# Optimization experiments

Hardware: AMD Instinct MI355X
Metric: run time of the kernel (lower is better)

The kernel has to match this reference:

```python
import jax, jax.numpy as jnp
import numpy as np

K = 8
W_CONST = 0.01
EPS = 1e-8


def _normalize(v, eps=1e-8):
    return v / (jnp.linalg.norm(v, axis=-1, keepdims=True) + eps)


def _coarse_normal(x, vertices, vertex_normals):
    # x: (N,3); vertices, vertex_normals: (V,3)
    # brute-force KNN (ascending by squared distance, like cKDTree.query)
    d2_all = jnp.sum((x[:, None, :] - vertices[None, :, :]) ** 2, axis=-1)  # (N,V)
    neg_d2, idx = jax.lax.top_k(-d2_all, K)  # sorted ascending distance
    d2 = -neg_d2                                                    # (N,K)
    v_knn = vertices[idx]                                           # (N,K,3)
    n_knn = vertex_normals[idx]                                     # (N,K,3)
    d2c = jnp.maximum(d2, EPS)
    inv_d2 = 1.0 / d2c                                              # (N,K)
    term_knn = jnp.sum(n_knn * inv_d2[..., None], axis=1)           # (N,3)
    v1 = v_knn[:, 0]                                                # nearest vertex
    d2_v1 = jnp.maximum(jnp.sum((x - v1) ** 2, axis=-1), EPS)       # (N,)
    term_dir = (x - v1) / (W_CONST * d2_v1[:, None])
    W = jnp.sum(inv_d2, axis=1) + 1.0 / W_CONST                     # (N,)
    n_tilde = (term_knn + term_dir) / W[:, None]
    nc = _normalize(n_tilde)
    return nc, v1


def _ray_mesh_first_hit(origins, dirs, tri0, e1, e2):
    # Moller-Trumbore, all points vs all faces. origins/dirs: (N,3); tri0/e1/e2: (F,3)
    pvec = jnp.cross(dirs[:, None, :], e2[None, :, :])              # (N,F,3)
    det = jnp.einsum('fk,nfk->nf', e1, pvec)                        # (N,F)
    ok_det = jnp.abs(det) > EPS
    inv_det = jnp.where(ok_det, 1.0 / jnp.where(ok_det, det, 1.0), 0.0)
    tvec = origins[:, None, :] - tri0[None, :, :]                   # (N,F,3)
    u = jnp.sum(tvec * pvec, axis=-1) * inv_det
    qvec = jnp.cross(tvec, e1[None, :, :])                          # (N,F,3)
    v = jnp.einsum('nk,nfk->nf', dirs, qvec) * inv_det
    t = jnp.einsum('fk,nfk->nf', e2, qvec) * inv_det
    valid = ok_det & (u >= 0.0) & (v >= 0.0) & (u + v <= 1.0) & (t > EPS)
    t_masked = jnp.where(valid, t, jnp.inf)
    t_min = jnp.min(t_masked, axis=1)                               # first hit along ray
    hit = jnp.isfinite(t_min)
    loc = origins + dirs * jnp.where(hit, t_min, 0.0)[:, None]
    return hit, loc


def _project(x, vertices, vertex_normals, faces):
    nc, v1 = _coarse_normal(x, vertices, vertex_normals)
    tri0 = vertices[faces[:, 0]]
    e1 = vertices[faces[:, 1]] - tri0
    e2 = vertices[faces[:, 2]] - tri0
    # primary cast along -nc
    hit1, loc1 = _ray_mesh_first_hit(x, -nc, tri0, e1, e2)
    # fallback cast toward nearest vertex
    dir_fb = _normalize(v1 - x)
    hit2, loc2 = _ray_mesh_first_hit(x, dir_fb, tri0, e1, e2)
    xc = jnp.where(hit1[:, None], loc1, jnp.where(hit2[:, None], loc2, v1))
    s = jnp.sum((x - xc) * nc, axis=-1, keepdims=True)              # (N,1)
    return xc, s, nc


def setup_inputs() -> dict:
    key = jax.random.key(0)
    k1, k2, k3, k4 = jax.random.split(key, 4)
    N, V, F = 2048, 8192, 8192
    x = jax.random.normal(k1, (N, 3), dtype=jnp.float32)
    vertices = jax.random.normal(k2, (V, 3), dtype=jnp.float32)
    vertex_normals = _normalize(jax.random.normal(k3, (V, 3), dtype=jnp.float32))
    faces = jax.random.randint(k4, (F, 3), 0, V, dtype=jnp.int32)
    return {"x": x, "vertices": vertices, "vertex_normals": vertex_normals, "faces": faces}


def reference(x, vertices, vertex_normals, faces):
    # returns (xc:(N,3), s:(N,1), nc:(N,3)) like ProjectionFn.forward
    return _project(x, vertices, vertex_normals, faces)
```

## Files before the change

kernel.cpp:

```cpp
#include <hip/hip_runtime.h>
#include <math.h>

#pragma float_control(precise, on)

#define EPSF 1e-8f
#define TRI_CHUNK 64


__global__ void __launch_bounds__(256) knn_kernel(
    const float* __restrict__ x, const float* __restrict__ verts,
    const float* __restrict__ vnorm, float* __restrict__ ncw,
    float* __restrict__ v1w, float* __restrict__ dfbw,
    unsigned int* __restrict__ tmin, int N, int V) {
#pragma clang fp contract(off)
    int p = blockIdx.x;
    int tid = threadIdx.x;
    int wave = tid >> 6;
    int lane = tid & 63;
    if (p >= N) return;

    if (tid < 2) tmin[2 * p + tid] = 0x7f800000u;

    float xx = x[p * 3 + 0];
    float xy = x[p * 3 + 1];
    float xz = x[p * 3 + 2];

    unsigned long long ka[8], kb[8];
#pragma unroll
    for (int i = 0; i < 8; ++i) { ka[i] = ~0ULL; kb[i] = ~0ULL; }

    for (int va = tid; va < V; va += 512) {
        int vb = va + 256;
        bool hasB = vb < V;

        float avx = verts[va * 3 + 0];
        float avy = verts[va * 3 + 1];
        float avz = verts[va * 3 + 2];
        float bvx = 0.f, bvy = 0.f, bvz = 0.f;
        if (hasB) {
            bvx = verts[vb * 3 + 0];
            bvy = verts[vb * 3 + 1];
            bvz = verts[vb * 3 + 2];
        }

        float dxa = xx - avx, dya = xy - avy, dza = xz - avz;
        float d2a = ((dxa * dxa) + (dya * dya)) + (dza * dza);
        unsigned long long kA =
            (((unsigned long long)__float_as_uint(d2a)) << 32) | (unsigned int)va;
        if (kA < ka[7]) {
            ka[7] = kA;
#pragma unroll
            for (int j = 7; j > 0; --j) {
                if (ka[j] < ka[j - 1]) {
                    unsigned long long t = ka[j];
                    ka[j] = ka[j - 1];
                    ka[j - 1] = t;
                }
            }
        }

        if (hasB) {
            float dxb = xx - bvx, dyb = xy - bvy, dzb = xz - bvz;
            float d2b = ((dxb * dxb) + (dyb * dyb)) + (dzb * dzb);
            unsigned long long kB =
                (((unsigned long long)__float_as_uint(d2b)) << 32) | (unsigned int)vb;
            if (kB < kb[7]) {
                kb[7] = kB;
#pragma unroll
                for (int j = 7; j > 0; --j) {
                    if (kb[j] < kb[j - 1]) {
                        unsigned long long t = kb[j];
                        kb[j] = kb[j - 1];
                        kb[j - 1] = t;
                    }
                }
            }
        }
    }

    unsigned long long wsel[8];
#pragma unroll
    for (int j = 0; j < 8; ++j) {
        unsigned long long c = (ka[0] < kb[0]) ? ka[0] : kb[0];
        unsigned long long m = c;
#pragma unroll
        for (int s = 1; s < 64; s <<= 1) {
            unsigned long long o = __shfl_xor(m, s, 64);
            if (o < m) m = o;
        }
        if (c == m) {
            if (ka[0] == m) {
#pragma unroll
                for (int t = 0; t < 7; ++t) ka[t] = ka[t + 1];
                ka[7] = ~0ULL;
            } else {
#pragma unroll
                for (int t = 0; t < 7; ++t) kb[t] = kb[t + 1];
                kb[7] = ~0ULL;
            }
        }
        wsel[j] = m;
    }

    __shared__ unsigned long long cand[32];
    if (lane == 0) {
#pragma unroll
        for (int j = 0; j < 8; ++j) cand[wave * 8 + j] = wsel[j];
    }
    __syncthreads();
    if (wave != 0) return;

    unsigned long long c0 = (lane < 32) ? cand[lane] : ~0ULL;
    unsigned long long sel[8];
#pragma unroll
    for (int j = 0; j < 8; ++j) {
        unsigned long long m = c0;
#pragma unroll
        for (int s = 1; s < 64; s <<= 1) {
            unsigned long long o = __shfl_xor(m, s, 64);
            if (o < m) m = o;
        }
        if (c0 == m) c0 = ~0ULL;
        sel[j] = m;
    }

    if (lane != 0) return;

    float invk[8];
    float nsx = 0.f, nsy = 0.f, nsz = 0.f;
#pragma unroll
    for (int j = 0; j < 8; ++j) {
        int id = (int)(sel[j] & 0xffffffffu);
        float d2 = __uint_as_float((unsigned int)(sel[j] >> 32));
        float inv = 1.0f / fmaxf(d2, EPSF);
        invk[j] = inv;
        nsx = nsx + vnorm[id * 3 + 0] * inv;
        nsy = nsy + vnorm[id * 3 + 1] * inv;
        nsz = nsz + vnorm[id * 3 + 2] * inv;
    }
    float Wsum = ((invk[0] + invk[1]) + (invk[2] + invk[3])) +
                 ((invk[4] + invk[5]) + (invk[6] + invk[7]));

    int id0 = (int)(sel[0] & 0xffffffffu);
    float v1x = verts[id0 * 3 + 0];
    float v1y = verts[id0 * 3 + 1];
    float v1z = verts[id0 * 3 + 2];

    float dxv = xx - v1x, dyv = xy - v1y, dzv = xz - v1z;
    float d2v1 = fmaxf(((dxv * dxv) + (dyv * dyv)) + (dzv * dzv), EPSF);
    float den = 0.01f * d2v1;
    float tdx = dxv / den, tdy = dyv / den, tdz = dzv / den;

    float W = Wsum + 100.0f;
    float ntx = (nsx + tdx) / W;
    float nty = (nsy + tdy) / W;
    float ntz = (nsz + tdz) / W;
    float nrm = sqrtf(((ntx * ntx) + (nty * nty)) + (ntz * ntz)) + 1e-8f;
    float ncx = ntx / nrm, ncy = nty / nrm, ncz = ntz / nrm;

    float fx = v1x - xx, fy = v1y - xy, fz = v1z - xz;
    float fn = sqrtf(((fx * fx) + (fy * fy)) + (fz * fz)) + 1e-8f;
    fx = fx / fn; fy = fy / fn; fz = fz / fn;

    ncw[p * 3 + 0] = ncx; ncw[p * 3 + 1] = ncy; ncw[p * 3 + 2] = ncz;
    v1w[p * 3 + 0] = v1x; v1w[p * 3 + 1] = v1y; v1w[p * 3 + 2] = v1z;
    dfbw[p * 3 + 0] = fx; dfbw[p * 3 + 1] = fy; dfbw[p * 3 + 2] = fz;
}

__global__ void __launch_bounds__(256) ray_kernel(
    const float* __restrict__ x, const float* __restrict__ ncw,
    const float* __restrict__ dfbw, const float* __restrict__ verts,
    const int* __restrict__ faces,
    unsigned int* __restrict__ tmin, int N, int F) {
#pragma clang fp contract(off)
    const float M = 1e-5f;
    __shared__ __align__(16) float sh[TRI_CHUNK * 12];
    int tid = threadIdx.x;
    int cbase = blockIdx.y * TRI_CHUNK;
    int cnt = min(TRI_CHUNK, F - cbase);

    for (int j = tid; j < cnt; j += 256) {
        int fi = cbase + j;
        int f0 = faces[fi * 3 + 0];
        int f1 = faces[fi * 3 + 1];
        int f2 = faces[fi * 3 + 2];
        float t0x = verts[f0 * 3 + 0], t0y = verts[f0 * 3 + 1], t0z = verts[f0 * 3 + 2];
        float ax = verts[f1 * 3 + 0], ay = verts[f1 * 3 + 1], az = verts[f1 * 3 + 2];
        float bx = verts[f2 * 3 + 0], by = verts[f2 * 3 + 1], bz = verts[f2 * 3 + 2];
        float4* s4 = (float4*)(sh + j * 12);
        s4[0] = make_float4(t0x, t0y, t0z, ax - t0x);
        s4[1] = make_float4(ay - t0y, az - t0z, bx - t0x, by - t0y);
        sh[j * 12 + 8] = bz - t0z;
    }
    __syncthreads();

    int rid = blockIdx.x * 256 + tid;
    if (rid >= 2 * N) return;
    int pnt = rid >> 1;

    float ox = x[pnt * 3 + 0];
    float oy = x[pnt * 3 + 1];
    float oz = x[pnt * 3 + 2];
    float dx, dy, dz;
    if (rid & 1) {
        dx = dfbw[pnt * 3 + 0]; dy = dfbw[pnt * 3 + 1]; dz = dfbw[pnt * 3 + 2];
    } else {
        dx = -ncw[pnt * 3 + 0]; dy = -ncw[pnt * 3 + 1]; dz = -ncw[pnt * 3 + 2];
    }

    const float INF = __uint_as_float(0x7f800000u);
    float tbest = INF;
    for (int j = 0; j < cnt; ++j) {
        const float4 A = *(const float4*)(sh + j * 12);
        const float4 B = *(const float4*)(sh + j * 12 + 4);
        const float e2z = sh[j * 12 + 8];
        float e1x = A.w, e1y = B.x, e1z = B.y;
        float e2x = B.z, e2y = B.w;
        float px = (dy * e2z) - (dz * e2y);
        float py = (dz * e2x) - (dx * e2z);
        float pz = (dx * e2y) - (dy * e2x);
        float det = ((e1x * px) + (e1y * py)) + (e1z * pz);
        bool ok = fabsf(det) > EPSF;
        float inv = ok ? (1.0f / det) : 0.0f;
        float tvx = ox - A.x;
        float tvy = oy - A.y;
        float tvz = oz - A.z;
        float u = (((tvx * px) + (tvy * py)) + (tvz * pz)) * inv;
        float qx = (tvy * e1z) - (tvz * e1y);
        float qy = (tvz * e1x) - (tvx * e1z);
        float qz = (tvx * e1y) - (tvy * e1x);
        float v = (((dx * qx) + (dy * qy)) + (dz * qz)) * inv;
        float t = (((e2x * qx) + (e2y * qy)) + (e2z * qz)) * inv;
        bool valid = ok && (u >= -M) && (v >= -M) && ((u + v) <= 1.0f + M) && (t > EPSF);
        tbest = (valid && t < tbest) ? t : tbest;
    }
    if (tbest < INF) atomicMin(&tmin[rid], __float_as_uint(tbest));
}

__global__ void finalize_kernel(const float* __restrict__ x,
                                const float* __restrict__ ncw,
                                const float* __restrict__ v1w,
                                const float* __restrict__ dfbw,
                                const unsigned int* __restrict__ tmin,
                                float* __restrict__ out, int N) {
#pragma clang fp contract(off)
    int p = blockIdx.x * blockDim.x + threadIdx.x;
    if (p >= N) return;
    float t1 = __uint_as_float(tmin[2 * p + 0]);
    float t2 = __uint_as_float(tmin[2 * p + 1]);
    bool h1 = t1 < __uint_as_float(0x7f800000u);
    bool h2 = t2 < __uint_as_float(0x7f800000u);

    float xx = x[p * 3 + 0], xy = x[p * 3 + 1], xz = x[p * 3 + 2];
    float ncx = ncw[p * 3 + 0], ncy = ncw[p * 3 + 1], ncz = ncw[p * 3 + 2];

    float xcx, xcy, xcz;
    if (h1) {
        xcx = xx + ((-ncx) * t1);
        xcy = xy + ((-ncy) * t1);
        xcz = xz + ((-ncz) * t1);
    } else if (h2) {
        xcx = xx + (dfbw[p * 3 + 0] * t2);
        xcy = xy + (dfbw[p * 3 + 1] * t2);
        xcz = xz + (dfbw[p * 3 + 2] * t2);
    } else {
        xcx = v1w[p * 3 + 0]; xcy = v1w[p * 3 + 1]; xcz = v1w[p * 3 + 2];
    }
    float s = (((xx - xcx) * ncx) + ((xy - xcy) * ncy)) + ((xz - xcz) * ncz);

    out[p * 3 + 0] = xcx;
    out[p * 3 + 1] = xcy;
    out[p * 3 + 2] = xcz;
    out[3 * N + p] = s;
    out[4 * N + p * 3 + 0] = ncx;
    out[4 * N + p * 3 + 1] = ncy;
    out[4 * N + p * 3 + 2] = ncz;
}

extern "C" void kernel_launch(void* const* d_in, const int* in_sizes, int n_in,
                              void* d_out, int out_size, void* d_ws, size_t ws_size,
                              hipStream_t stream) {
    const float* x     = (const float*)d_in[0];
    const float* verts = (const float*)d_in[1];
    const float* vnorm = (const float*)d_in[2];
    const int*   faces = (const int*)d_in[3];
    int N = in_sizes[0] / 3;
    int V = in_sizes[1] / 3;
    int F = in_sizes[3] / 3;

    unsigned int* tmin = (unsigned int*)d_ws;
    float* ncw  = (float*)(tmin + 2 * N);
    float* v1w  = ncw + 3 * N;
    float* dfbw = v1w + 3 * N;

    hipLaunchKernelGGL(knn_kernel, dim3(N), dim3(256), 0, stream,
                       x, verts, vnorm, ncw, v1w, dfbw, tmin, N, V);
    int chunks = (F + TRI_CHUNK - 1) / TRI_CHUNK;
    int rblocks = (2 * N + 255) / 256;
    hipLaunchKernelGGL(ray_kernel, dim3(rblocks, chunks), dim3(256), 0, stream,
                       x, ncw, dfbw, verts, faces, tmin, N, F);
    hipLaunchKernelGGL(finalize_kernel, dim3((N + 255) / 256), dim3(256), 0, stream,
                       x, ncw, v1w, dfbw, tmin, (float*)d_out, N);
}
```

Baseline: 157.9 us.

## Process both rays per point in one thread, sharing tvec and qvec work

Each thread now handles one point and tests both of its rays (primary and fallback) against every triangle in the chunk. The direction-independent tvec, qvec and the t numerator are computed once and reused for both rays, and shared-memory triangle loads are amortized over two rays. The triangle chunk is halved to keep the block count up, and a launch-bounds occupancy hint is added. In exchange each thread uses more registers, there are more chunks and atomics overall, and only half as many threads work per chunk.

```diff
diff --git a/kernel.cpp b/kernel.cpp
--- a/kernel.cpp
+++ b/kernel.cpp
@@ -4,7 +4,7 @@
 #pragma float_control(precise, on)
 
 #define EPSF 1e-8f
-#define TRI_CHUNK 64
+#define TRI_CHUNK 32
 
 
 __global__ void __launch_bounds__(256) knn_kernel(
@@ -167,7 +167,7 @@
     dfbw[p * 3 + 0] = fx; dfbw[p * 3 + 1] = fy; dfbw[p * 3 + 2] = fz;
 }
 
-__global__ void __launch_bounds__(256) ray_kernel(
+__global__ void __launch_bounds__(256, 4) ray_kernel(
     const float* __restrict__ x, const float* __restrict__ ncw,
     const float* __restrict__ dfbw, const float* __restrict__ verts,
     const int* __restrict__ faces,
@@ -194,47 +194,61 @@
     }
     __syncthreads();
 
-    int rid = blockIdx.x * 256 + tid;
-    if (rid >= 2 * N) return;
-    int pnt = rid >> 1;
+    int pnt = blockIdx.x * 256 + tid;
+    if (pnt >= N) return;
 
     float ox = x[pnt * 3 + 0];
     float oy = x[pnt * 3 + 1];
     float oz = x[pnt * 3 + 2];
-    float dx, dy, dz;
-    if (rid & 1) {
-        dx = dfbw[pnt * 3 + 0]; dy = dfbw[pnt * 3 + 1]; dz = dfbw[pnt * 3 + 2];
-    } else {
-        dx = -ncw[pnt * 3 + 0]; dy = -ncw[pnt * 3 + 1]; dz = -ncw[pnt * 3 + 2];
-    }
+    float dax = -ncw[pnt * 3 + 0], day = -ncw[pnt * 3 + 1], daz = -ncw[pnt * 3 + 2];
+    float dbx = dfbw[pnt * 3 + 0], dby = dfbw[pnt * 3 + 1], dbz = dfbw[pnt * 3 + 2];
 
     const float INF = __uint_as_float(0x7f800000u);
-    float tbest = INF;
+    float tba = INF, tbb = INF;
     for (int j = 0; j < cnt; ++j) {
         const float4 A = *(const float4*)(sh + j * 12);
         const float4 B = *(const float4*)(sh + j * 12 + 4);
         const float e2z = sh[j * 12 + 8];
         float e1x = A.w, e1y = B.x, e1z = B.y;
         float e2x = B.z, e2y = B.w;
-        float px = (dy * e2z) - (dz * e2y);
-        float py = (dz * e2x) - (dx * e2z);
-        float pz = (dx * e2y) - (dy * e2x);
-        float det = ((e1x * px) + (e1y * py)) + (e1z * pz);
-        bool ok = fabsf(det) > EPSF;
-        float inv = ok ? (1.0f / det) : 0.0f;
+
         float tvx = ox - A.x;
         float tvy = oy - A.y;
         float tvz = oz - A.z;
-        float u = (((tvx * px) + (tvy * py)) + (tvz * pz)) * inv;
         float qx = (tvy * e1z) - (tvz * e1y);
         float qy = (tvz * e1x) - (tvx * e1z);
         float qz = (tvx * e1y) - (tvy * e1x);
-        float v = (((dx * qx) + (dy * qy)) + (dz * qz)) * inv;
-        float t = (((e2x * qx) + (e2y * qy)) + (e2z * qz)) * inv;
-        bool valid = ok && (u >= -M) && (v >= -M) && ((u + v) <= 1.0f + M) && (t > EPSF);
-        tbest = (valid && t < tbest) ? t : tbest;
-    }
-    if (tbest < INF) atomicMin(&tmin[rid], __float_as_uint(tbest));
+        float tq = ((e2x * qx) + (e2y * qy)) + (e2z * qz);
+
+        {
+            float px = (day * e2z) - (daz * e2y);
+            float py = (daz * e2x) - (dax * e2z);
+            float pz = (dax * e2y) - (day * e2x);
+            float det = ((e1x * px) + (e1y * py)) + (e1z * pz);
+            bool ok = fabsf(det) > EPSF;
+            float inv = ok ? (1.0f / det) : 0.0f;
+            float u = (((tvx * px) + (tvy * py)) + (tvz * pz)) * inv;
+            float v = (((dax * qx) + (day * qy)) + (daz * qz)) * inv;
+            float t = tq * inv;
+            bool valid = ok && (u >= -M) && (v >= -M) && ((u + v) <= 1.0f + M) && (t > EPSF);
+            tba = (valid && t < tba) ? t : tba;
+        }
+        {
+            float px = (dby * e2z) - (dbz * e2y);
+            float py = (dbz * e2x) - (dbx * e2z);
+            float pz = (dbx * e2y) - (dby * e2x);
+            float det = ((e1x * px) + (e1y * py)) + (e1z * pz);
+            bool ok = fabsf(det) > EPSF;
+            float inv = ok ? (1.0f / det) : 0.0f;
+            float u = (((tvx * px) + (tvy * py)) + (tvz * pz)) * inv;
+            float v = (((dbx * qx) + (dby * qy)) + (dbz * qz)) * inv;
+            float t = tq * inv;
+            bool valid = ok && (u >= -M) && (v >= -M) && ((u + v) <= 1.0f + M) && (t > EPSF);
+            tbb = (valid && t < tbb) ? t : tbb;
+        }
+    }
+    if (tba < INF) atomicMin(&tmin[2 * pnt + 0], __float_as_uint(tba));
+    if (tbb < INF) atomicMin(&tmin[2 * pnt + 1], __float_as_uint(tbb));
 }
 
 __global__ void finalize_kernel(const float* __restrict__ x,
@@ -296,8 +310,8 @@
     hipLaunchKernelGGL(knn_kernel, dim3(N), dim3(256), 0, stream,
                        x, verts, vnorm, ncw, v1w, dfbw, tmin, N, V);
     int chunks = (F + TRI_CHUNK - 1) / TRI_CHUNK;
-    int rblocks = (2 * N + 255) / 256;
-    hipLaunchKernelGGL(ray_kernel, dim3(rblocks, chunks), dim3(256), 0, stream,
+    int pblocks = (N + 255) / 256;
+    hipLaunchKernelGGL(ray_kernel, dim3(pblocks, chunks), dim3(256), 0, stream,
                        x, ncw, dfbw, verts, faces, tmin, N, F);
     hipLaunchKernelGGL(finalize_kernel, dim3((N + 255) / 256), dim3(256), 0, stream,
                        x, ncw, v1w, dfbw, tmin, (float*)d_out, N);
```

Result: faster. 145.4 us (-8.0%).
